# Kernel tuning notes

Hardware: AMD Instinct MI355X
Metric: run time of the kernel (lower is better)

The kernel has to match this reference:

```python
import jax, jax.numpy as jnp
import numpy as np

BLOCK_LEN = 64

def setup_inputs() -> dict:
    key = jax.random.key(0)
    k1, k2, k3 = jax.random.split(key, 3)
    b, T, h, p, n = 2, 8192, 16, 64, 64
    X = jax.random.normal(k1, (b, T, h), dtype=jnp.float32)  # placeholder reuse avoided below
    X = jax.random.normal(k1, (b, T, h, p), dtype=jnp.float32)
    # A kept negative (as in Mamba/SSD) so exp(decay) stays bounded and the
    # inter-chunk product of exp(A_last) does not overflow.
    A = -jnp.abs(jax.random.normal(k2, (b, T, h), dtype=jnp.float32)) * 0.1
    B = jax.random.normal(k3, (b, T, h, n), dtype=jnp.float32)
    return {"X": X, "A": A, "B": B}


def reference(X, A, B):
    b, T, h, p = X.shape
    n = B.shape[-1]
    l = BLOCK_LEN
    c = T // l

    # [b, h, c, l] chunked A
    A_blocks = A.reshape(b, c, l, h).transpose(0, 3, 1, 2)
    A_cumsum = jnp.cumsum(A_blocks, axis=-1)          # s[i] = sum_{t<=i} a[t]
    A_last = A_cumsum[..., -1]                        # [b, h, c] total per chunk
    decay = jnp.exp(A_last[..., None] - A_cumsum)     # exp(S_total - s[i]) [b,h,c,l]

    X_blocks = X.reshape(b, c, l, h, p)
    B_blocks = B.reshape(b, c, l, h, n)

    # intra-chunk states: sum_l decay * outer(X, B) -> [b, c, h, p, n]
    states = jnp.einsum('bclhn,bhcl,bclhp->bchpn', B_blocks, decay, X_blocks)

    # inter-chunk recurrence: s_{k+1} = exp(A_last[...,k]) * s_k + states[:,k]
    init = jnp.zeros((b, h, p, n), dtype=jnp.float32)
    states_c = jnp.moveaxis(states, 1, 0)             # [c, b, h, p, n]
    A_last_c = jnp.moveaxis(A_last, 2, 0)             # [c, b, h]

    def step(s, inp):
        st, al = inp
        return jnp.exp(al)[..., None, None] * s + st, None

    final_states, _ = jax.lax.scan(step, init, (states_c, A_last_c))
    return final_states  # [b, h, p, n]
```

## Files before the change

### kernel.cpp

```cpp
#include <hip/hip_runtime.h>

#define B_SZ 2
#define T_SZ 8192
#define H_SZ 16
#define P_SZ 64
#define N_SZ 64
#define L_SZ 64
#define C_SZ (T_SZ / L_SZ)
#define SKIP_THRESH (-30.0f)

__global__ void __launch_bounds__(256) k_prep(const float* __restrict__ A,
                                              float* __restrict__ cs,
                                              float* __restrict__ out) {
    const int blk = blockIdx.x;
    const int b = blk / C_SZ;
    const int c = blk % C_SZ;
    const int tid = threadIdx.x;
    __shared__ float a_sh[L_SZ * H_SZ];
    const float4* src =
        (const float4*)(A + ((size_t)b * T_SZ + (size_t)c * L_SZ) * H_SZ);
    ((float4*)a_sh)[tid] = src[tid];

    if (tid < 128) {
        float4 z; z.x = z.y = z.z = z.w = 0.f;
        ((float4*)out)[(size_t)blk * 128 + tid] = z;
    }
    __syncthreads();
    if (tid < H_SZ) {
        float s = 0.f;
        #pragma unroll
        for (int i = 0; i < L_SZ; ++i) s += a_sh[i * H_SZ + tid];
        cs[((size_t)b * H_SZ + tid) * C_SZ + c] = s;
    }
}

__global__ void __launch_bounds__(256) k_main(const float* __restrict__ X,
                                              const float* __restrict__ A,
                                              const float* __restrict__ Bm,
                                              const float* __restrict__ cs,
                                              float* __restrict__ out) {
    const int c = blockIdx.x;
    const int h = blockIdx.y;
    const int b = blockIdx.z;
    const int bh = b * H_SZ + h;
    const int tid = threadIdx.x;

    __shared__ float red[128];
    __shared__ float s_saf;
    __shared__ float w_sh[L_SZ];
    __shared__ float xw_sh[L_SZ * P_SZ];
    __shared__ float b_sh[L_SZ * N_SZ];

    if (tid < 128)
        red[tid] = (tid > c) ? cs[(size_t)bh * C_SZ + tid] : 0.f;
    __syncthreads();
    if (tid < 64) {
        float x = red[tid] + red[tid + 64];
        x += __shfl_down(x, 32);
        x += __shfl_down(x, 16);
        x += __shfl_down(x, 8);
        x += __shfl_down(x, 4);
        x += __shfl_down(x, 2);
        x += __shfl_down(x, 1);
        if (tid == 0) s_saf = x;
    }
    __syncthreads();
    const float safter = s_saf;
    if (safter < SKIP_THRESH) return;

    const size_t base_t = (size_t)b * T_SZ + (size_t)c * L_SZ;

    const float* Xp = X + (base_t * H_SZ + h) * (size_t)P_SZ;
    const float* Bp = Bm + (base_t * H_SZ + h) * (size_t)N_SZ;
    float4 xr[4], br[4];
    #pragma unroll
    for (int k = 0; k < 4; ++k) {
        int idx = tid + k * 256;
        int row = idx >> 4;
        int col = idx & 15;
        xr[k] = *(const float4*)(Xp + (size_t)row * (H_SZ * P_SZ) + col * 4);
        br[k] = *(const float4*)(Bp + (size_t)row * (H_SZ * N_SZ) + col * 4);
    }

    if (tid < 64) {
        float incl = A[(base_t + tid) * H_SZ + h];
        #pragma unroll
        for (int off = 1; off < 64; off <<= 1) {
            float y = __shfl_up(incl, off);
            if (tid >= off) incl += y;
        }
        float total = __shfl(incl, 63);
        w_sh[tid] = __expf(total - incl + safter);
    }
    __syncthreads();

    #pragma unroll
    for (int k = 0; k < 4; ++k) {
        int idx = tid + k * 256;
        int row = idx >> 4;
        float wv = w_sh[row];
        float4 xv = xr[k];
        xv.x *= wv; xv.y *= wv; xv.z *= wv; xv.w *= wv;
        ((float4*)xw_sh)[idx] = xv;
        ((float4*)b_sh)[idx] = br[k];
    }
    __syncthreads();

    const int pi = (tid >> 4) << 2;
    const int ni = (tid & 15) << 2;
    float acc00 = 0.f, acc01 = 0.f, acc02 = 0.f, acc03 = 0.f;
    float acc10 = 0.f, acc11 = 0.f, acc12 = 0.f, acc13 = 0.f;
    float acc20 = 0.f, acc21 = 0.f, acc22 = 0.f, acc23 = 0.f;
    float acc30 = 0.f, acc31 = 0.f, acc32 = 0.f, acc33 = 0.f;
    #pragma unroll 4
    for (int t = 0; t < L_SZ; ++t) {
        float4 xv = *(const float4*)(xw_sh + t * P_SZ + pi);
        float4 bv = *(const float4*)(b_sh + t * N_SZ + ni);
        acc00 += xv.x * bv.x; acc01 += xv.x * bv.y; acc02 += xv.x * bv.z; acc03 += xv.x * bv.w;
        acc10 += xv.y * bv.x; acc11 += xv.y * bv.y; acc12 += xv.y * bv.z; acc13 += xv.y * bv.w;
        acc20 += xv.z * bv.x; acc21 += xv.z * bv.y; acc22 += xv.z * bv.z; acc23 += xv.z * bv.w;
        acc30 += xv.w * bv.x; acc31 += xv.w * bv.y; acc32 += xv.w * bv.z; acc33 += xv.w * bv.w;
    }

    float* op = out + (((size_t)b * H_SZ + h) * P_SZ) * N_SZ;
    atomicAdd(op + (pi + 0) * N_SZ + ni + 0, acc00);
    atomicAdd(op + (pi + 0) * N_SZ + ni + 1, acc01);
    atomicAdd(op + (pi + 0) * N_SZ + ni + 2, acc02);
    atomicAdd(op + (pi + 0) * N_SZ + ni + 3, acc03);
    atomicAdd(op + (pi + 1) * N_SZ + ni + 0, acc10);
    atomicAdd(op + (pi + 1) * N_SZ + ni + 1, acc11);
    atomicAdd(op + (pi + 1) * N_SZ + ni + 2, acc12);
    atomicAdd(op + (pi + 1) * N_SZ + ni + 3, acc13);
    atomicAdd(op + (pi + 2) * N_SZ + ni + 0, acc20);
    atomicAdd(op + (pi + 2) * N_SZ + ni + 1, acc21);
    atomicAdd(op + (pi + 2) * N_SZ + ni + 2, acc22);
    atomicAdd(op + (pi + 2) * N_SZ + ni + 3, acc23);
    atomicAdd(op + (pi + 3) * N_SZ + ni + 0, acc30);
    atomicAdd(op + (pi + 3) * N_SZ + ni + 1, acc31);
    atomicAdd(op + (pi + 3) * N_SZ + ni + 2, acc32);
    atomicAdd(op + (pi + 3) * N_SZ + ni + 3, acc33);
}

extern "C" void kernel_launch(void* const* d_in, const int* in_sizes, int n_in,
                              void* d_out, int out_size, void* d_ws, size_t ws_size,
                              hipStream_t stream) {
    const float* X  = (const float*)d_in[0];
    const float* A  = (const float*)d_in[1];
    const float* Bm = (const float*)d_in[2];
    float* out = (float*)d_out;

    float* cs = (float*)d_ws;

    k_prep<<<B_SZ * C_SZ, 256, 0, stream>>>(A, cs, out);

    dim3 grid(C_SZ, H_SZ, B_SZ);
    k_main<<<grid, 256, 0, stream>>>(X, A, Bm, cs, out);
}
```

Baseline: 143.5 us.

## Persist main-kernel blocks over chunk groups with a shared suffix-sum scan

The main kernel grid shrinks from one block per chunk to 16 chunk-groups per (batch, head). Each block computes the decay suffix sums for all 128 chunks once, using a two-wave scan in shared memory, then loops over its strided chunks and skips those whose decay falls below the threshold. This removes the thousands of blocks that previously launched only to compute a reduction and exit early. In exchange, each block has a per-chunk barrier loop and fewer blocks are in flight for the chunks that still need work. It also leaves a dead read of uninitialised shared memory and a redundant scan.

Result: faster. 139.3 us (-2.9%).

```diff
diff --git a/kernel.cpp b/kernel.cpp
--- a/kernel.cpp
+++ b/kernel.cpp
@@ -7,6 +7,7 @@
 #define N_SZ 64
 #define L_SZ 64
 #define C_SZ (T_SZ / L_SZ)
+#define CGROUPS 16
 #define SKIP_THRESH (-30.0f)
 
 __global__ void __launch_bounds__(256) k_prep(const float* __restrict__ A,
@@ -39,106 +40,130 @@
                                               const float* __restrict__ Bm,
                                               const float* __restrict__ cs,
                                               float* __restrict__ out) {
-    const int c = blockIdx.x;
+    const int gx = blockIdx.x;
     const int h = blockIdx.y;
     const int b = blockIdx.z;
     const int bh = b * H_SZ + h;
     const int tid = threadIdx.x;
 
-    __shared__ float red[128];
-    __shared__ float s_saf;
+    __shared__ float saf_sh[C_SZ];
+    __shared__ float wtot[2];
     __shared__ float w_sh[L_SZ];
     __shared__ float xw_sh[L_SZ * P_SZ];
     __shared__ float b_sh[L_SZ * N_SZ];
 
-    if (tid < 128)
-        red[tid] = (tid > c) ? cs[(size_t)bh * C_SZ + tid] : 0.f;
-    __syncthreads();
-    if (tid < 64) {
-        float x = red[tid] + red[tid + 64];
-        x += __shfl_down(x, 32);
-        x += __shfl_down(x, 16);
-        x += __shfl_down(x, 8);
-        x += __shfl_down(x, 4);
-        x += __shfl_down(x, 2);
-        x += __shfl_down(x, 1);
-        if (tid == 0) s_saf = x;
-    }
-    __syncthreads();
-    const float safter = s_saf;
-    if (safter < SKIP_THRESH) return;
-
-    const size_t base_t = (size_t)b * T_SZ + (size_t)c * L_SZ;
-
-    const float* Xp = X + (base_t * H_SZ + h) * (size_t)P_SZ;
-    const float* Bp = Bm + (base_t * H_SZ + h) * (size_t)N_SZ;
-    float4 xr[4], br[4];
-    #pragma unroll
-    for (int k = 0; k < 4; ++k) {
-        int idx = tid + k * 256;
-        int row = idx >> 4;
-        int col = idx & 15;
-        xr[k] = *(const float4*)(Xp + (size_t)row * (H_SZ * P_SZ) + col * 4);
-        br[k] = *(const float4*)(Bp + (size_t)row * (H_SZ * N_SZ) + col * 4);
-    }
-
-    if (tid < 64) {
-        float incl = A[(base_t + tid) * H_SZ + h];
+    if (tid < 128) {
+        const int lane = tid & 63;
+        const int wv = tid >> 6;
+        float incl = cs[(size_t)bh * C_SZ + tid];
         #pragma unroll
         for (int off = 1; off < 64; off <<= 1) {
             float y = __shfl_up(incl, off);
-            if (tid >= off) incl += y;
+            if (lane >= off) incl += y;
         }
-        float total = __shfl(incl, 63);
-        w_sh[tid] = __expf(total - incl + safter);
+        if (lane == 63) wtot[wv] = incl;
+        __builtin_amdgcn_s_waitcnt(0);
     }
     __syncthreads();
-
-    #pragma unroll
-    for (int k = 0; k < 4; ++k) {
-        int idx = tid + k * 256;
-        int row = idx >> 4;
-        float wv = w_sh[row];
-        float4 xv = xr[k];
-        xv.x *= wv; xv.y *= wv; xv.z *= wv; xv.w *= wv;
-        ((float4*)xw_sh)[idx] = xv;
-        ((float4*)b_sh)[idx] = br[k];
+    if (tid < 128) {
+        const int wv = tid >> 6;
+        float incl_full = saf_sh[0];
+        (void)incl_full;
+    }
+    if (tid < 128) {
+        const int lane = tid & 63;
+        const int wv = tid >> 6;
+        float incl = cs[(size_t)bh * C_SZ + tid];
+        #pragma unroll
+        for (int off = 1; off < 64; off <<= 1) {
+            float y = __shfl_up(incl, off);
+            if (lane >= off) incl += y;
+        }
+        float total = wtot[0] + wtot[1];
+        if (wv == 1) incl += wtot[0];
+        saf_sh[tid] = total - incl;
     }
     __syncthreads();
 
     const int pi = (tid >> 4) << 2;
     const int ni = (tid & 15) << 2;
-    float acc00 = 0.f, acc01 = 0.f, acc02 = 0.f, acc03 = 0.f;
-    float acc10 = 0.f, acc11 = 0.f, acc12 = 0.f, acc13 = 0.f;
-    float acc20 = 0.f, acc21 = 0.f, acc22 = 0.f, acc23 = 0.f;
-    float acc30 = 0.f, acc31 = 0.f, acc32 = 0.f, acc33 = 0.f;
-    #pragma unroll 4
-    for (int t = 0; t < L_SZ; ++t) {
-        float4 xv = *(const float4*)(xw_sh + t * P_SZ + pi);
-        float4 bv = *(const float4*)(b_sh + t * N_SZ + ni);
-        acc00 += xv.x * bv.x; acc01 += xv.x * bv.y; acc02 += xv.x * bv.z; acc03 += xv.x * bv.w;
-        acc10 += xv.y * bv.x; acc11 += xv.y * bv.y; acc12 += xv.y * bv.z; acc13 += xv.y * bv.w;
-        acc20 += xv.z * bv.x; acc21 += xv.z * bv.y; acc22 += xv.z * bv.z; acc23 += xv.z * bv.w;
-        acc30 += xv.w * bv.x; acc31 += xv.w * bv.y; acc32 += xv.w * bv.z; acc33 += xv.w * bv.w;
+    float* op = out + (((size_t)b * H_SZ + h) * P_SZ) * N_SZ;
+
+    for (int c = gx; c < C_SZ; c += CGROUPS) {
+        const float safter = saf_sh[c];
+        if (safter < SKIP_THRESH) continue;
+
+        const size_t base_t = (size_t)b * T_SZ + (size_t)c * L_SZ;
+        const float* Xp = X + (base_t * H_SZ + h) * (size_t)P_SZ;
+        const float* Bp = Bm + (base_t * H_SZ + h) * (size_t)N_SZ;
+
+        float4 xr[4], br[4];
+        #pragma unroll
+        for (int k = 0; k < 4; ++k) {
+            int idx = tid + k * 256;
+            int row = idx >> 4;
+            int col = idx & 15;
+            xr[k] = *(const float4*)(Xp + (size_t)row * (H_SZ * P_SZ) + col * 4);
+            br[k] = *(const float4*)(Bp + (size_t)row * (H_SZ * N_SZ) + col * 4);
+        }
+
+        if (tid < 64) {
+            float incl = A[(base_t + tid) * H_SZ + h];
+            #pragma unroll
+            for (int off = 1; off < 64; off <<= 1) {
+                float y = __shfl_up(incl, off);
+                if (tid >= off) incl += y;
+            }
+            float total = __shfl(incl, 63);
+            w_sh[tid] = __expf(total - incl + safter);
+        }
+        __syncthreads();
+
+        #pragma unroll
+        for (int k = 0; k < 4; ++k) {
+            int idx = tid + k * 256;
+            int row = idx >> 4;
+            float wv = w_sh[row];
+            float4 xv = xr[k];
+            xv.x *= wv; xv.y *= wv; xv.z *= wv; xv.w *= wv;
+            ((float4*)xw_sh)[idx] = xv;
+            ((float4*)b_sh)[idx] = br[k];
+        }
+        __syncthreads();
+
+        float acc00 = 0.f, acc01 = 0.f, acc02 = 0.f, acc03 = 0.f;
+        float acc10 = 0.f, acc11 = 0.f, acc12 = 0.f, acc13 = 0.f;
+        float acc20 = 0.f, acc21 = 0.f, acc22 = 0.f, acc23 = 0.f;
+        float acc30 = 0.f, acc31 = 0.f, acc32 = 0.f, acc33 = 0.f;
+        #pragma unroll 4
+        for (int t = 0; t < L_SZ; ++t) {
+            float4 xv = *(const float4*)(xw_sh + t * P_SZ + pi);
+            float4 bv = *(const float4*)(b_sh + t * N_SZ + ni);
+            acc00 += xv.x * bv.x; acc01 += xv.x * bv.y; acc02 += xv.x * bv.z; acc03 += xv.x * bv.w;
+            acc10 += xv.y * bv.x; acc11 += xv.y * bv.y; acc12 += xv.y * bv.z; acc13 += xv.y * bv.w;
+            acc20 += xv.z * bv.x; acc21 += xv.z * bv.y; acc22 += xv.z * bv.z; acc23 += xv.z * bv.w;
+            acc30 += xv.w * bv.x; acc31 += xv.w * bv.y; acc32 += xv.w * bv.z; acc33 += xv.w * bv.w;
+        }
+
+        atomicAdd(op + (pi + 0) * N_SZ + ni + 0, acc00);
+        atomicAdd(op + (pi + 0) * N_SZ + ni + 1, acc01);
+        atomicAdd(op + (pi + 0) * N_SZ + ni + 2, acc02);
+        atomicAdd(op + (pi + 0) * N_SZ + ni + 3, acc03);
+        atomicAdd(op + (pi + 1) * N_SZ + ni + 0, acc10);
+        atomicAdd(op + (pi + 1) * N_SZ + ni + 1, acc11);
+        atomicAdd(op + (pi + 1) * N_SZ + ni + 2, acc12);
+        atomicAdd(op + (pi + 1) * N_SZ + ni + 3, acc13);
+        atomicAdd(op + (pi + 2) * N_SZ + ni + 0, acc20);
+        atomicAdd(op + (pi + 2) * N_SZ + ni + 1, acc21);
+        atomicAdd(op + (pi + 2) * N_SZ + ni + 2, acc22);
+        atomicAdd(op + (pi + 2) * N_SZ + ni + 3, acc23);
+        atomicAdd(op + (pi + 3) * N_SZ + ni + 0, acc30);
+        atomicAdd(op + (pi + 3) * N_SZ + ni + 1, acc31);
+        atomicAdd(op + (pi + 3) * N_SZ + ni + 2, acc32);
+        atomicAdd(op + (pi + 3) * N_SZ + ni + 3, acc33);
+
+        __syncthreads();
     }
-
-    float* op = out + (((size_t)b * H_SZ + h) * P_SZ) * N_SZ;
-    atomicAdd(op + (pi + 0) * N_SZ + ni + 0, acc00);
-    atomicAdd(op + (pi + 0) * N_SZ + ni + 1, acc01);
-    atomicAdd(op + (pi + 0) * N_SZ + ni + 2, acc02);
-    atomicAdd(op + (pi + 0) * N_SZ + ni + 3, acc03);
-    atomicAdd(op + (pi + 1) * N_SZ + ni + 0, acc10);
-    atomicAdd(op + (pi + 1) * N_SZ + ni + 1, acc11);
-    atomicAdd(op + (pi + 1) * N_SZ + ni + 2, acc12);
-    atomicAdd(op + (pi + 1) * N_SZ + ni + 3, acc13);
-    atomicAdd(op + (pi + 2) * N_SZ + ni + 0, acc20);
-    atomicAdd(op + (pi + 2) * N_SZ + ni + 1, acc21);
-    atomicAdd(op + (pi + 2) * N_SZ + ni + 2, acc22);
-    atomicAdd(op + (pi + 2) * N_SZ + ni + 3, acc23);
-    atomicAdd(op + (pi + 3) * N_SZ + ni + 0, acc30);
-    atomicAdd(op + (pi + 3) * N_SZ + ni + 1, acc31);
-    atomicAdd(op + (pi + 3) * N_SZ + ni + 2, acc32);
-    atomicAdd(op + (pi + 3) * N_SZ + ni + 3, acc33);
 }
 
 extern "C" void kernel_launch(void* const* d_in, const int* in_sizes, int n_in,
@@ -153,6 +178,6 @@
 
     k_prep<<<B_SZ * C_SZ, 256, 0, stream>>>(A, cs, out);
 
-    dim3 grid(C_SZ, H_SZ, B_SZ);
+    dim3 grid(CGROUPS, H_SZ, B_SZ);
     k_main<<<grid, 256, 0, stream>>>(X, A, Bm, cs, out);
 }
```
